# Performance work log

Measured on AMD Instinct MI355X. Metric: run time of the kernel, lower is better.

Reference implementation:

```python
import jax, jax.numpy as jnp
import numpy as np

FEAT_DIM = 16
NUM_DEPTHS = 64


def _lookat(p):
    z = p / np.linalg.norm(p)
    up = np.array([0.0, 1.0, 0.0])
    x = np.cross(up, z); x = x / np.linalg.norm(x)
    y = np.cross(z, x)
    m = np.eye(4)
    m[:3, 0] = x; m[:3, 1] = y; m[:3, 2] = z; m[:3, 3] = p
    return m


def setup_inputs() -> dict:
    key = jax.random.key(0)
    ks = jax.random.split(key, 6)
    S, Vin, Vt, C, D, H, W = 2, 3, 4, FEAT_DIM, NUM_DEPTHS, 96, 96
    enc = jax.random.normal(ks[0], (S, Vin, C, D, H, W), jnp.float32) * 0.5
    rng = np.random.default_rng(0)

    def poses(n):
        ps = rng.normal(size=(S, n, 3))
        ps = ps / np.linalg.norm(ps, axis=-1, keepdims=True) * 1.3
        return jnp.asarray(np.stack([[_lookat(ps[i, j]) for j in range(n)] for i in range(S)]), jnp.float32)

    input_poses = poses(Vin)
    target_poses = poses(Vt)
    W1 = jax.random.normal(ks[1], (16, 64), jnp.float32) * 0.25
    W2 = jax.random.normal(ks[2], (64, 64), jnp.float32) * 0.125
    W3 = jax.random.normal(ks[3], (64, 17), jnp.float32) * 0.125
    return dict(
        encoded_imgs=enc, input_poses=input_poses, target_poses=target_poses,
        focal=1.2, z_near=0.8, z_far=1.8, samples_per_ray=64,
        W1=W1, b1=jnp.zeros((64,), jnp.float32),
        W2=W2, b2=jnp.zeros((64,), jnp.float32),
        W3=W3, b3=jnp.zeros((17,), jnp.float32),
    )


def grid_sample_3d(vol, grid):
    # vol: (N,C,D,H,W); grid: (N,P,3) xyz in [-1,1]; trilinear, zero padding, align_corners=False
    N, C, D, H, W = vol.shape
    P = grid.shape[1]
    ix = ((grid[..., 0] + 1.0) * W - 1.0) * 0.5
    iy = ((grid[..., 1] + 1.0) * H - 1.0) * 0.5
    iz = ((grid[..., 2] + 1.0) * D - 1.0) * 0.5
    x0, y0, z0 = jnp.floor(ix), jnp.floor(iy), jnp.floor(iz)
    volf = vol.reshape(N, C, D * H * W)
    out = jnp.zeros((N, C, P), vol.dtype)
    for dz in (0, 1):
        for dy in (0, 1):
            for dx in (0, 1):
                xc, yc, zc = x0 + dx, y0 + dy, z0 + dz
                wgt = (1.0 - jnp.abs(ix - xc)) * (1.0 - jnp.abs(iy - yc)) * (1.0 - jnp.abs(iz - zc))
                valid = ((xc >= 0) & (xc < W) & (yc >= 0) & (yc < H) & (zc >= 0) & (zc < D))
                xi = jnp.clip(xc, 0, W - 1).astype(jnp.int32)
                yi = jnp.clip(yc, 0, H - 1).astype(jnp.int32)
                zi = jnp.clip(zc, 0, D - 1).astype(jnp.int32)
                idx = (zi * H + yi) * W + xi  # (N,P)
                vals = jnp.take_along_axis(volf, idx[:, None, :], axis=2)  # (N,C,P)
                out = out + (wgt * valid)[:, None, :] * vals
    return out


def _upsample2_align_corners(x):
    # bilinear x2 on last two axes, align_corners=True (torch UpsamplingBilinear2d)
    def interp(x, axis):
        n = x.shape[axis]
        m = 2 * n
        pos = jnp.arange(m) * ((n - 1) / (m - 1))
        lo = jnp.floor(pos).astype(jnp.int32)
        hi = jnp.minimum(lo + 1, n - 1)
        f = (pos - lo).astype(x.dtype)
        xl = jnp.take(x, lo, axis=axis)
        xh = jnp.take(x, hi, axis=axis)
        shp = [1] * x.ndim; shp[axis] = m
        f = f.reshape(shp)
        return xl * (1.0 - f) + xh * f
    return interp(interp(x, -2), -1)


def _forward(encoded_imgs, input_poses, target_poses, focal, z_near, z_far,
             samples_per_ray, W1, b1, W2, b2, W3, b3):
    S, Vin, C, D, H, W = encoded_imgs.shape
    Vt = target_poses.shape[1]
    h, w = H // 2, W // 2
    spr = samples_per_ray
    dt = encoded_imgs.dtype

    # --- gen_rays at half resolution ---
    poses = target_poses.reshape(S * Vt, 4, 4)
    ys = ((jnp.arange(h, dtype=dt) + 0.5) / h) * 2.0 - 1.0
    xs = ((jnp.arange(w, dtype=dt) + 0.5) / w) * 2.0 - 1.0
    yy, xx = jnp.meshgrid(ys, xs, indexing='ij')
    dirs_cam = jnp.stack([xx / focal, -yy / focal, -jnp.ones_like(xx)], -1)  # (h,w,3)
    dirs = jnp.einsum('bij,hwj->bhwi', poses[:, :3, :3], dirs_cam)            # (B,h,w,3)
    origins = poses[:, None, None, :3, 3]                                      # (B,1,1,3)

    t = z_near + (z_far - z_near) * (jnp.arange(spr, dtype=dt) / (spr - 1))
    times = jnp.broadcast_to(t, (S * Vt, h, w, spr))
    pts = origins[..., None, :] + times[..., None] * dirs[..., None, :]        # (B,h,w,spr,3)

    times = times.reshape(S, Vt, h, w, spr)
    pts = pts.reshape(S, Vt, h, w, spr, 3)
    pts_h = jnp.concatenate([pts, jnp.ones_like(pts[..., :1])], axis=-1)      # (S,Vt,h,w,spr,4)

    # --- invert input poses (rigid) ---
    R = input_poses[..., :3, :3]
    tr = input_poses[..., :3, 3]
    Rt = jnp.swapaxes(R, -1, -2)
    inv_t = -jnp.einsum('svij,svj->svi', Rt, tr)
    top = jnp.concatenate([Rt, inv_t[..., None]], axis=-1)                     # (S,Vin,3,4)
    bottom = jnp.broadcast_to(jnp.array([0.0, 0.0, 0.0, 1.0], dt), (S, Vin, 1, 4))
    extrinsics = jnp.concatenate([top, bottom], axis=-2)                       # (S,Vin,4,4)

    local = jnp.einsum('svij,sthwpj->svthwpi', extrinsics, pts_h)              # (S,Vin,Vt,h,w,spr,4)
    x = local[..., 0]
    y = local[..., 1]
    z = -local[..., 2]
    u = x / z * focal
    v = y / z * focal
    min_z, max_z = focal * z_near, focal * z_far
    wd = 2.0 * (z - min_z) / (max_z - min_z) - 1.0
    uvw = jnp.stack((u, -v, -wd), axis=-1)                                     # (S,Vin,Vt,h,w,spr,3)

    feats = grid_sample_3d(encoded_imgs.reshape(S * Vin, C, D, H, W),
                           uvw.reshape(S * Vin, -1, 3))                        # (S*Vin,C,P)
    feats = feats.reshape(S, Vin, C, Vt, h, w, spr)
    feats = jnp.mean(feats, axis=1)                                            # baseline_mean camera weighting
    feats = jnp.transpose(feats, (0, 2, 3, 4, 5, 1))                           # (S,Vt,h,w,spr,C)

    # --- MLP with residual feature skip ---
    x1 = jax.nn.relu(feats @ W1 + b1)
    x2 = jax.nn.relu(x1 @ W2 + b2)
    out = x2 @ W3 + b3                                                         # (...,17)
    density = jax.nn.relu(out[..., 0])
    rgb = feats + out[..., 1:]

    # --- volume rendering ---
    deltas = times[..., 1:] - times[..., :-1]
    last = jnp.full_like(deltas[..., :1], 1e10)
    deltas = jnp.concatenate([deltas, last], axis=-1)
    sigdel = density * deltas
    alpha = 1.0 - jnp.exp(-sigdel)
    transmittance = jnp.exp(-jnp.cumsum(sigdel, axis=-1))
    wts = alpha * transmittance
    renders = jnp.sum(wts[..., None] * rgb, axis=-2)                           # (S,Vt,h,w,16)

    renders = jnp.transpose(renders, (0, 1, 4, 2, 3))                          # (S,Vt,16,h,w)
    renders = _upsample2_align_corners(renders.reshape(S * Vt, C, h, w))
    return renders.reshape(S, Vt, C, H, W)


def reference(encoded_imgs, input_poses, target_poses, focal, z_near, z_far,
              samples_per_ray, W1, b1, W2, b2, W3, b3):
    return _forward(encoded_imgs, input_poses, target_poses, float(focal), float(z_near),
                    float(z_far), int(samples_per_ray), W1, b1, W2, b2, W3, b3)
```

## Files before the change

### kernel.cpp

```cpp
#include <hip/hip_runtime.h>
#include <hip/hip_bf16.h>
#include <math.h>

#define NS   2
#define NVIN 3
#define NVT  4
#define NC   16
#define ND   64
#define NH   96
#define NW   96
#define HWH  48
#define SPR  64
#define DHW  (ND*NH*NW)
#define NTILE (DHW / 64)
#define NSAMP (NS*NVT*HWH*HWH*SPR)
#define NRAYS (NS*NVT*HWH*HWH)

typedef __attribute__((ext_vector_type(8))) short bfrag;
typedef __attribute__((ext_vector_type(4))) float cfrag;
typedef __attribute__((ext_vector_type(4))) float f32x4;
typedef __attribute__((ext_vector_type(4))) int   i32x4;

#define MFMA16 __builtin_amdgcn_mfma_f32_16x16x32_bf16

#define WAVE_LDS_SYNC() asm volatile("s_waitcnt lgkmcnt(0)" ::: "memory")

__device__ __forceinline__ short f2bf(float x) {
    union { __hip_bfloat16 b; short s; } cv;
    cv.b = __float2bfloat16(x);
    return cv.s;
}
__device__ __forceinline__ float bf2f(short s) {
    union { unsigned int u; float f; } cv;
    cv.u = ((unsigned int)(unsigned short)s) << 16;
    return cv.f;
}

__device__ __forceinline__ void mk_frag(const float* p, bfrag& ah, bfrag& al) {
    float4 v0 = *(const float4*)p;
    float4 v1 = *(const float4*)(p + 4);
    float e[8] = {v0.x, v0.y, v0.z, v0.w, v1.x, v1.y, v1.z, v1.w};
    #pragma unroll
    for (int j = 0; j < 8; j++) {
        short h = f2bf(e[j]);
        ah[j] = h;
        al[j] = f2bf(e[j] - bf2f(h));
    }
}

__global__ __launch_bounds__(256) void wprep_kernel(
    const float* __restrict__ W1, const float* __restrict__ W2,
    const float* __restrict__ W3, short* __restrict__ whi, short* __restrict__ wlo)
{
    int t = blockIdx.x * 256 + threadIdx.x;
    int f = t >> 6, L = t & 63;
    int q = L >> 4, li = L & 15;
    #pragma unroll
    for (int j = 0; j < 8; j++) {
        int kloc = q * 8 + j;
        float w = 0.f;
        if (f < 4) {
            int n = f * 16 + li, k = kloc;
            if (k < 16) w = W1[k * 64 + n];
        } else if (f < 12) {
            int kt = (f - 4) >> 2, nt = (f - 4) & 3;
            w = W2[(kt * 32 + kloc) * 64 + nt * 16 + li];
        } else {
            int kt = (f - 12) >> 1, nt = (f - 12) & 1;
            int n = nt * 16 + li;
            if (n < 17) w = W3[(kt * 32 + kloc) * 17 + n];
        }
        short h = f2bf(w);
        whi[(f * 64 + L) * 8 + j] = h;
        wlo[(f * 64 + L) * 8 + j] = f2bf(w - bf2f(h));
    }
}

__global__ __launch_bounds__(256) void transpose_kernel(
    const float* __restrict__ in, float* __restrict__ out)
{
    __shared__ float tile[NC][64 + 4];
    const int t   = threadIdx.x;
    const int blk = blockIdx.x;
    const int vox0 = (blk % NTILE) * 64;
    const int sv   = blk / NTILE;

    const int c  = t >> 4;
    const int vg = (t & 15) * 4;
    const float* src = in + ((size_t)sv * NC + c) * DHW + vox0 + vg;
    float4 v = *(const float4*)src;
    tile[c][vg + 0] = v.x; tile[c][vg + 1] = v.y;
    tile[c][vg + 2] = v.z; tile[c][vg + 3] = v.w;
    __syncthreads();

    const int ov = t >> 2;
    const int oc = (t & 3) * 4;
    float4 w = make_float4(tile[oc + 0][ov], tile[oc + 1][ov],
                           tile[oc + 2][ov], tile[oc + 3][ov]);
    float* dst = out + ((size_t)sv * DHW + vox0 + ov) * NC + oc;
    *(float4*)dst = w;
}

__global__ __launch_bounds__(256) void gather_kernel(
    const float* __restrict__ enc_t,
    const float* __restrict__ ipose,
    const float* __restrict__ tpose,
    const float* __restrict__ focal_p,
    const float* __restrict__ znear_p,
    const float* __restrict__ zfar_p,
    float* __restrict__ xbuf)
{
    const int blk  = (blockIdx.x & 7) * ((NRAYS / 4) >> 3) + (blockIdx.x >> 3);
    const int lane = threadIdx.x & 63;
    const int wv   = threadIdx.x >> 6;
    const int ray  = blk * 4 + wv;
    const int px   = ray % HWH;
    const int py   = (ray / HWH) % HWH;
    const int b    = ray / (HWH * HWH);
    const int s    = b >> 2;

    const float focal = focal_p[0];
    const float znear = znear_p[0];
    const float zfar  = zfar_p[0];

    __shared__ float lds[4 * 32 * 52];
    float* wslice = lds + wv * 32 * 52;

    const float* P = tpose + b * 16;
    float ysc = ((py + 0.5f) / (float)HWH) * 2.f - 1.f;
    float xsc = ((px + 0.5f) / (float)HWH) * 2.f - 1.f;
    float dcx = xsc / focal, dcy = -ysc / focal, dcz = -1.f;
    float dirx = P[0]*dcx + P[1]*dcy + P[2]*dcz;
    float diry = P[4]*dcx + P[5]*dcy + P[6]*dcz;
    float dirz = P[8]*dcx + P[9]*dcy + P[10]*dcz;

    float lox[NVIN], loy[NVIN], loz[NVIN];
    float ldx[NVIN], ldy[NVIN], ldz[NVIN];
    #pragma unroll
    for (int v = 0; v < NVIN; v++) {
        const float* E = ipose + (s * NVIN + v) * 16;
        float qx = P[3] - E[3], qy = P[7] - E[7], qz = P[11] - E[11];
        lox[v] = E[0]*qx + E[4]*qy + E[8]*qz;
        loy[v] = E[1]*qx + E[5]*qy + E[9]*qz;
        loz[v] = E[2]*qx + E[6]*qy + E[10]*qz;
        ldx[v] = E[0]*dirx + E[4]*diry + E[8]*dirz;
        ldy[v] = E[1]*dirx + E[5]*diry + E[9]*dirz;
        ldz[v] = E[2]*dirx + E[6]*diry + E[10]*dirz;
    }

    const float minz = focal * znear, maxz = focal * zfar;
    const float inv3 = 1.f / 3.f;
    const int c4 = lane & 3;
    const int cb = c4 * 16;

    #pragma unroll 1
    for (int h = 0; h < 2; h++) {
        WAVE_LDS_SYNC();

        if (lane < 32) {
            const int d = h * 32 + lane;
            float tv = znear + (zfar - znear) * ((float)d / (float)(SPR - 1));
            float* row = wslice + lane * 52;
            #pragma unroll
            for (int v = 0; v < NVIN; v++) {
                float lx = lox[v] + tv * ldx[v];
                float ly = loy[v] + tv * ldy[v];
                float lz = loz[v] + tv * ldz[v];
                float zz = -lz;
                float u  = lx / zz * focal;
                float vv = ly / zz * focal;
                float wd = 2.f * (zz - minz) / (maxz - minz) - 1.f;
                float ix = ((u   + 1.f) * NW - 1.f) * 0.5f;
                float iy = ((-vv + 1.f) * NH - 1.f) * 0.5f;
                float iz = ((-wd + 1.f) * ND - 1.f) * 0.5f;
                float x0 = floorf(ix), y0 = floorf(iy), z0 = floorf(iz);
                float x1 = x0 + 1.f,   y1 = y0 + 1.f,   z1 = z0 + 1.f;

                float wxa0 = 1.f - fabsf(ix - x0), wxa1 = 1.f - fabsf(ix - x1);
                float wya0 = 1.f - fabsf(iy - y0), wya1 = 1.f - fabsf(iy - y1);
                float wza0 = 1.f - fabsf(iz - z0), wza1 = 1.f - fabsf(iz - z1);
                wxa0 = (x0 >= 0.f && x0 < (float)NW) ? wxa0 : 0.f;
                wxa1 = (x1 >= 0.f && x1 < (float)NW) ? wxa1 : 0.f;
                wya0 = (y0 >= 0.f && y0 < (float)NH) ? wya0 : 0.f;
                wya1 = (y1 >= 0.f && y1 < (float)NH) ? wya1 : 0.f;
                wza0 = (z0 >= 0.f && z0 < (float)ND) ? wza0 : 0.f;
                wza1 = (z1 >= 0.f && z1 < (float)ND) ? wza1 : 0.f;

                int xi0 = min(max((int)x0, 0), NW - 1), xi1 = min(max((int)x1, 0), NW - 1);
                int yi0 = min(max((int)y0, 0), NH - 1), yi1 = min(max((int)y1, 0), NH - 1);
                int zi0 = min(max((int)z0, 0), ND - 1), zi1 = min(max((int)z1, 0), ND - 1);
                int o00 = (zi0 * NH + yi0) * NW, o01 = (zi0 * NH + yi1) * NW;
                int o10 = (zi1 * NH + yi0) * NW, o11 = (zi1 * NH + yi1) * NW;

                const int sb = (s * NVIN + v) * (DHW * NC * 4);

                f32x4 w0 = { (wxa0*wya0)*wza0, (wxa1*wya0)*wza0,
                             (wxa0*wya1)*wza0, (wxa1*wya1)*wza0 };
                f32x4 w1 = { (wxa0*wya0)*wza1, (wxa1*wya0)*wza1,
                             (wxa0*wya1)*wza1, (wxa1*wya1)*wza1 };
                i32x4 o0 = { sb + (o00 + xi0) * 64, sb + (o00 + xi1) * 64,
                             sb + (o01 + xi0) * 64, sb + (o01 + xi1) * 64 };
                i32x4 o1 = { sb + (o10 + xi0) * 64, sb + (o10 + xi1) * 64,
                             sb + (o11 + xi0) * 64, sb + (o11 + xi1) * 64 };

                *(f32x4*)(row + v*16 + 0)  = w0;
                *(f32x4*)(row + v*16 + 4)  = w1;
                *(i32x4*)(row + v*16 + 8)  = o0;
                *(i32x4*)(row + v*16 + 12) = o1;
            }
        }
        WAVE_LDS_SYNC();

        #pragma unroll 1
        for (int pass = 0; pass < 2; pass++) {
            const int sl = pass * 16 + (lane >> 2);
            const float* row = wslice + sl * 52;
            f32x4 acc = {0.f, 0.f, 0.f, 0.f};

            #pragma unroll
            for (int v = 0; v < NVIN; v++) {
                f32x4 wq0 = *(const f32x4*)(row + v*16 + 0);
                f32x4 wq1 = *(const f32x4*)(row + v*16 + 4);
                i32x4 oq0 = *(const i32x4*)(row + v*16 + 8);
                i32x4 oq1 = *(const i32x4*)(row + v*16 + 12);

                f32x4 a0, a1, a2, a3, a4, a5, a6, a7;
                int v0 = oq0.x + cb, v1 = oq0.y + cb, v2 = oq0.z + cb, v3 = oq0.w + cb;
                int v4 = oq1.x + cb, v5 = oq1.y + cb, v6 = oq1.z + cb, v7 = oq1.w + cb;
                asm volatile("global_load_dwordx4 %0, %1, %2" : "=&v"(a0) : "v"(v0), "s"(enc_t));
                asm volatile("global_load_dwordx4 %0, %1, %2" : "=&v"(a1) : "v"(v1), "s"(enc_t));
                asm volatile("global_load_dwordx4 %0, %1, %2" : "=&v"(a2) : "v"(v2), "s"(enc_t));
                asm volatile("global_load_dwordx4 %0, %1, %2" : "=&v"(a3) : "v"(v3), "s"(enc_t));
                asm volatile("global_load_dwordx4 %0, %1, %2" : "=&v"(a4) : "v"(v4), "s"(enc_t));
                asm volatile("global_load_dwordx4 %0, %1, %2" : "=&v"(a5) : "v"(v5), "s"(enc_t));
                asm volatile("global_load_dwordx4 %0, %1, %2" : "=&v"(a6) : "v"(v6), "s"(enc_t));
                asm volatile("global_load_dwordx4 %0, %1, %2" : "=&v"(a7) : "v"(v7), "s"(enc_t));
                asm volatile("s_waitcnt vmcnt(0)" ::: "memory");
                __builtin_amdgcn_sched_barrier(0);

                acc += wq0.x * a0;  acc += wq0.y * a1;
                acc += wq0.z * a2;  acc += wq0.w * a3;
                acc += wq1.x * a4;  acc += wq1.y * a5;
                acc += wq1.z * a6;  acc += wq1.w * a7;
            }
            ((f32x4*)xbuf)[(ray * 64 + h * 32 + sl) * 4 + c4] = acc * inv3;
        }
    }
}

__global__ __launch_bounds__(64) void mlp_kernel(
    const float* __restrict__ xbuf,
    const float* __restrict__ znear_p,
    const float* __restrict__ zfar_p,
    const short* __restrict__ whi, const short* __restrict__ wlo,
    const float* __restrict__ B1, const float* __restrict__ B2,
    const float* __restrict__ B3,
    float* __restrict__ rhalf)
{
    const int lane = threadIdx.x & 63;
    const int ray  = blockIdx.x;
    const int px   = ray % HWH;
    const int py   = (ray / HWH) % HWH;
    const int b    = ray / (HWH * HWH);

    const float znear = znear_p[0];
    const float zfar  = zfar_p[0];

    __shared__ float sbuf[64][36];
    float (*B)[36] = sbuf;
    const int li = lane & 15, q = lane >> 4;
    const float* X = xbuf + (size_t)ray * 64 * NC;

    float b1v[4], b2v[4], b3v[2];
    #pragma unroll
    for (int nt = 0; nt < 4; nt++) { b1v[nt] = B1[nt*16 + li]; b2v[nt] = B2[nt*16 + li]; }
    b3v[0] = B3[li];
    b3v[1] = (li == 0) ? B3[16] : 0.f;

    bfrag xah[4], xal[4];
    bfrag zb = {0,0,0,0,0,0,0,0};
    #pragma unroll
    for (int mt = 0; mt < 4; mt++) {
        if (q < 2) mk_frag(X + (mt*16 + li) * NC + q * 8, xah[mt], xal[mt]);
        else { xah[mt] = zb; xal[mt] = zb; }
    }

    cfrag zc = {0.f, 0.f, 0.f, 0.f};
    cfrag h2acc[4][4];
    #pragma unroll
    for (int mt = 0; mt < 4; mt++)
        #pragma unroll
        for (int nt = 0; nt < 4; nt++) h2acc[mt][nt] = zc;

    #pragma unroll
    for (int c1 = 0; c1 < 2; c1++) {
        cfrag h1[4][2];
        #pragma unroll
        for (int nt2 = 0; nt2 < 2; nt2++) {
            int f = 2*c1 + nt2;
            bfrag bh = *(const bfrag*)(whi + (f*64 + lane)*8);
            bfrag bl = *(const bfrag*)(wlo + (f*64 + lane)*8);
            #pragma unroll
            for (int mt = 0; mt < 4; mt++) {
                cfrag a = zc;
                a = MFMA16(xal[mt], bh, a, 0, 0, 0);
                a = MFMA16(xah[mt], bl, a, 0, 0, 0);
                a = MFMA16(xah[mt], bh, a, 0, 0, 0);
                h1[mt][nt2] = a;
            }
        }
        WAVE_LDS_SYNC();
        #pragma unroll
        for (int mt = 0; mt < 4; mt++)
            #pragma unroll
            for (int nt2 = 0; nt2 < 2; nt2++)
                #pragma unroll
                for (int r = 0; r < 4; r++)
                    B[mt*16 + q*4 + r][nt2*16 + li] =
                        fmaxf(h1[mt][nt2][r] + b1v[2*c1 + nt2], 0.f);
        WAVE_LDS_SYNC();
        bfrag hah[4], hal[4];
        #pragma unroll
        for (int mt = 0; mt < 4; mt++)
            mk_frag(&B[mt*16 + li][q*8], hah[mt], hal[mt]);
        #pragma unroll
        for (int nt = 0; nt < 4; nt++) {
            int f = 4 + c1*4 + nt;
            bfrag bh = *(const bfrag*)(whi + (f*64 + lane)*8);
            bfrag bl = *(const bfrag*)(wlo + (f*64 + lane)*8);
            #pragma unroll
            for (int mt = 0; mt < 4; mt++) {
                cfrag a = h2acc[mt][nt];
                a = MFMA16(hal[mt], bh, a, 0, 0, 0);
                a = MFMA16(hah[mt], bl, a, 0, 0, 0);
                a = MFMA16(hah[mt], bh, a, 0, 0, 0);
                h2acc[mt][nt] = a;
            }
        }
    }

    cfrag oacc[4][2];
    #pragma unroll
    for (int mt = 0; mt < 4; mt++)
        #pragma unroll
        for (int nt = 0; nt < 2; nt++) oacc[mt][nt] = zc;

    #pragma unroll
    for (int c2 = 0; c2 < 2; c2++) {
        WAVE_LDS_SYNC();
        #pragma unroll
        for (int mt = 0; mt < 4; mt++)
            #pragma unroll
            for (int nt2 = 0; nt2 < 2; nt2++)
                #pragma unroll
                for (int r = 0; r < 4; r++)
                    B[mt*16 + q*4 + r][nt2*16 + li] =
                        fmaxf(h2acc[mt][2*c2 + nt2][r] + b2v[2*c2 + nt2], 0.f);
        WAVE_LDS_SYNC();
        bfrag hah[4], hal[4];
        #pragma unroll
        for (int mt = 0; mt < 4; mt++)
            mk_frag(&B[mt*16 + li][q*8], hah[mt], hal[mt]);
        #pragma unroll
        for (int nt = 0; nt < 2; nt++) {
            int f = 12 + c2*2 + nt;
            bfrag bh = *(const bfrag*)(whi + (f*64 + lane)*8);
            bfrag bl = *(const bfrag*)(wlo + (f*64 + lane)*8);
            #pragma unroll
            for (int mt = 0; mt < 4; mt++) {
                cfrag a = oacc[mt][nt];
                a = MFMA16(hal[mt], bh, a, 0, 0, 0);
                a = MFMA16(hah[mt], bl, a, 0, 0, 0);
                a = MFMA16(hah[mt], bh, a, 0, 0, 0);
                oacc[mt][nt] = a;
            }
        }
    }

    WAVE_LDS_SYNC();
    #pragma unroll
    for (int mt = 0; mt < 4; mt++)
        #pragma unroll
        for (int nt = 0; nt < 2; nt++) {
            int ch = nt*16 + li;
            if (ch < 17) {
                #pragma unroll
                for (int r = 0; r < 4; r++)
                    B[mt*16 + q*4 + r][ch] = oacc[mt][nt][r] + b3v[nt];
            }
        }
    WAVE_LDS_SYNC();
    float4 o0 = *(float4*)&B[lane][0];
    float4 o1 = *(float4*)&B[lane][4];
    float4 o2 = *(float4*)&B[lane][8];
    float4 o3 = *(float4*)&B[lane][12];
    float o16 = B[lane][16];

    float density = fmaxf(o0.x, 0.f);
    float orgb[16] = {o0.y, o0.z, o0.w, o1.x, o1.y, o1.z, o1.w, o2.x,
                      o2.y, o2.z, o2.w, o3.x, o3.y, o3.z, o3.w, o16};

    float4 fx0 = *(const float4*)(X + lane * NC + 0);
    float4 fx1 = *(const float4*)(X + lane * NC + 4);
    float4 fx2 = *(const float4*)(X + lane * NC + 8);
    float4 fx3 = *(const float4*)(X + lane * NC + 12);
    float feats[16] = {fx0.x, fx0.y, fx0.z, fx0.w, fx1.x, fx1.y, fx1.z, fx1.w,
                       fx2.x, fx2.y, fx2.z, fx2.w, fx3.x, fx3.y, fx3.z, fx3.w};

    float tv = znear + (zfar - znear) * ((float)lane / (float)(SPR - 1));
    float tn = znear + (zfar - znear) * ((float)(lane + 1) / (float)(SPR - 1));
    float delta = (lane < SPR - 1) ? (tn - tv) : 1e10f;
    float sigdel = density * delta;
    float alpha = 1.f - expf(-sigdel);
    float csum = sigdel;
    #pragma unroll
    for (int off = 1; off < 64; off <<= 1) {
        float nb = __shfl_up(csum, off, 64);
        if (lane >= off) csum += nb;
    }
    float wray = alpha * expf(-csum);

    #pragma unroll
    for (int c = 0; c < NC; c++) {
        float val = wray * (feats[c] + orgb[c]);
        #pragma unroll
        for (int off = 32; off >= 1; off >>= 1)
            val += __shfl_down(val, off, 64);
        if (lane == 0)
            rhalf[((b * NC + c) * HWH + py) * HWH + px] = val;
    }
}

__device__ __forceinline__ void mlp_and_composite(
    const float feats[NC], int lane, int b, int py, int px,
    float tv, float znear, float zfar,
    const float* __restrict__ W1, const float* __restrict__ B1,
    const float* __restrict__ W2, const float* __restrict__ B2,
    const float* __restrict__ W3, const float* __restrict__ B3,
    float* __restrict__ rhalf)
{
    float outa[17];
    #pragma unroll
    for (int c = 0; c < 17; c++) outa[c] = B3[c];
    for (int kc = 0; kc < 4; kc++) {
        float h2c[16];
        #pragma unroll
        for (int k = 0; k < 16; k++) h2c[k] = B2[kc * 16 + k];
        #pragma unroll 4
        for (int j = 0; j < 64; j++) {
            float a = B1[j];
            #pragma unroll
            for (int i = 0; i < NC; i++) a += feats[i] * W1[i * 64 + j];
            a = fmaxf(a, 0.f);
            const float* w2p = W2 + j * 64 + kc * 16;
            #pragma unroll
            for (int k = 0; k < 16; k++) h2c[k] += a * w2p[k];
        }
        #pragma unroll
        for (int k = 0; k < 16; k++) {
            float hv = fmaxf(h2c[k], 0.f);
            const float* w3p = W3 + (kc * 16 + k) * 17;
            #pragma unroll
            for (int c = 0; c < 17; c++) outa[c] += hv * w3p[c];
        }
    }
    float density = fmaxf(outa[0], 0.f);
    float tn = znear + (zfar - znear) * ((float)(lane + 1) / (float)(SPR - 1));
    float delta = (lane < SPR - 1) ? (tn - tv) : 1e10f;
    float sigdel = density * delta;
    float alpha = 1.f - expf(-sigdel);
    float csum = sigdel;
    #pragma unroll
    for (int off = 1; off < 64; off <<= 1) {
        float nb = __shfl_up(csum, off, 64);
        if (lane >= off) csum += nb;
    }
    float wray = alpha * expf(-csum);
    #pragma unroll
    for (int c = 0; c < NC; c++) {
        float val = wray * (feats[c] + outa[1 + c]);
        #pragma unroll
        for (int off = 32; off >= 1; off >>= 1)
            val += __shfl_down(val, off, 64);
        if (lane == 0)
            rhalf[((b * NC + c) * HWH + py) * HWH + px] = val;
    }
}

__global__ __launch_bounds__(256) void render_kernel(
    const float* __restrict__ enc,
    const float* __restrict__ ipose,
    const float* __restrict__ tpose,
    const float* __restrict__ focal_p,
    const float* __restrict__ znear_p,
    const float* __restrict__ zfar_p,
    const float* __restrict__ W1, const float* __restrict__ B1,
    const float* __restrict__ W2, const float* __restrict__ B2,
    const float* __restrict__ W3, const float* __restrict__ B3,
    float* __restrict__ rhalf)
{
    const int lane = threadIdx.x & 63;
    const int ray  = blockIdx.x * 4 + (threadIdx.x >> 6);
    const int px   = ray % HWH;
    const int py   = (ray / HWH) % HWH;
    const int b    = ray / (HWH * HWH);
    const int s    = b >> 2;
    const float focal = focal_p[0];
    const float znear = znear_p[0];
    const float zfar  = zfar_p[0];
    const float* P = tpose + b * 16;
    float ysc = ((py + 0.5f) / (float)HWH) * 2.f - 1.f;
    float xsc = ((px + 0.5f) / (float)HWH) * 2.f - 1.f;
    float dcx = xsc / focal, dcy = -ysc / focal, dcz = -1.f;
    float dirx = P[0]*dcx + P[1]*dcy + P[2]*dcz;
    float diry = P[4]*dcx + P[5]*dcy + P[6]*dcz;
    float dirz = P[8]*dcx + P[9]*dcy + P[10]*dcz;
    float tv  = znear + (zfar - znear) * ((float)lane / (float)(SPR - 1));
    float ptx = P[3] + tv * dirx, pty = P[7] + tv * diry, ptz = P[11] + tv * dirz;
    float feats[NC];
    #pragma unroll
    for (int c = 0; c < NC; c++) feats[c] = 0.f;
    const float minz = focal * znear, maxz = focal * zfar;
    for (int v = 0; v < NVIN; v++) {
        const float* E = ipose + (s * NVIN + v) * 16;
        float qx = ptx - E[3], qy = pty - E[7], qz = ptz - E[11];
        float lx = E[0]*qx + E[4]*qy + E[8]*qz;
        float ly = E[1]*qx + E[5]*qy + E[9]*qz;
        float lz = E[2]*qx + E[6]*qy + E[10]*qz;
        float zz = -lz;
        float u  = lx / zz * focal;
        float vv = ly / zz * focal;
        float wd = 2.f * (zz - minz) / (maxz - minz) - 1.f;
        float ix = ((u   + 1.f) * NW - 1.f) * 0.5f;
        float iy = ((-vv + 1.f) * NH - 1.f) * 0.5f;
        float iz = ((-wd + 1.f) * ND - 1.f) * 0.5f;
        float x0 = floorf(ix), y0 = floorf(iy), z0 = floorf(iz);
        float wgt[8]; int idx[8];
        #pragma unroll
        for (int k = 0; k < 8; k++) {
            float xc = x0 + (k & 1), yc = y0 + ((k >> 1) & 1), zc = z0 + (k >> 2);
            float wt = (1.f - fabsf(ix - xc)) * (1.f - fabsf(iy - yc)) * (1.f - fabsf(iz - zc));
            bool valid = (xc >= 0.f) && (xc < (float)NW) &&
                         (yc >= 0.f) && (yc < (float)NH) &&
                         (zc >= 0.f) && (zc < (float)ND);
            wgt[k] = valid ? wt : 0.f;
            int xi = min(max((int)xc, 0), NW - 1);
            int yi = min(max((int)yc, 0), NH - 1);
            int zi = min(max((int)zc, 0), ND - 1);
            idx[k] = (zi * NH + yi) * NW + xi;
        }
        const float* VB = enc + (size_t)(s * NVIN + v) * NC * DHW;
        #pragma unroll
        for (int c = 0; c < NC; c++) {
            const float* vc = VB + c * DHW;
            float acc = 0.f;
            #pragma unroll
            for (int k = 0; k < 8; k++) acc += wgt[k] * vc[idx[k]];
            feats[c] += acc;
        }
    }
    #pragma unroll
    for (int c = 0; c < NC; c++) feats[c] *= (1.f / 3.f);
    mlp_and_composite(feats, lane, b, py, px, tv, znear, zfar,
                      W1, B1, W2, B2, W3, B3, rhalf);
}

__global__ __launch_bounds__(256) void upsample_kernel(
    const float* __restrict__ in, float* __restrict__ out)
{
    int tid = blockIdx.x * 256 + threadIdx.x;
    int ox = tid % NW;
    int oy = (tid / NW) % NH;
    int c  = (tid / (NW * NH)) % NC;
    int b  = tid / (NW * NH * NC);
    const float sc = (float)((HWH - 1) / (double)(NH - 1));
    float pyf = oy * sc;
    float pxf = ox * sc;
    int y0 = (int)floorf(pyf); int y1 = min(y0 + 1, HWH - 1); float fy = pyf - y0;
    int x0 = (int)floorf(pxf); int x1 = min(x0 + 1, HWH - 1); float fx = pxf - x0;
    const float* src = in + (b * NC + c) * HWH * HWH;
    float v00 = src[y0 * HWH + x0], v01 = src[y0 * HWH + x1];
    float v10 = src[y1 * HWH + x0], v11 = src[y1 * HWH + x1];
    float gl = v00 * (1.f - fy) + v10 * fy;
    float gr = v01 * (1.f - fy) + v11 * fy;
    out[tid] = gl * (1.f - fx) + gr * fx;
}

extern "C" void kernel_launch(void* const* d_in, const int* in_sizes, int n_in,
                              void* d_out, int out_size, void* d_ws, size_t ws_size,
                              hipStream_t stream) {
    const float* enc   = (const float*)d_in[0];
    const float* ipose = (const float*)d_in[1];
    const float* tpose = (const float*)d_in[2];
    const float* focal = (const float*)d_in[3];
    const float* znear = (const float*)d_in[4];
    const float* zfar  = (const float*)d_in[5];
    const float* W1 = (const float*)d_in[7];
    const float* B1 = (const float*)d_in[8];
    const float* W2 = (const float*)d_in[9];
    const float* B2 = (const float*)d_in[10];
    const float* W3 = (const float*)d_in[11];
    const float* B3 = (const float*)d_in[12];

    float* out = (float*)d_out;
    const int nrays = NRAYS;
    const int nout  = NS * NVT * NC * NH * NW;
    const size_t enc_t_bytes = (size_t)NS * NVIN * NC * DHW * 4;
    const size_t rhalf_bytes = (size_t)nrays * NC * 4;
    const size_t wfrag_bytes = 16 * 64 * 8 * sizeof(short);
    const size_t xbuf_bytes  = (size_t)NSAMP * NC * 4;

    if (ws_size >= enc_t_bytes + rhalf_bytes + 2 * wfrag_bytes + xbuf_bytes) {
        char* base = (char*)d_ws;
        float* enc_t = (float*)base;                      base += enc_t_bytes;
        float* rhalf = (float*)base;                      base += rhalf_bytes;
        short* whi   = (short*)base;                      base += wfrag_bytes;
        short* wlo   = (short*)base;                      base += wfrag_bytes;
        float* xbuf  = (float*)base;

        wprep_kernel<<<4, 256, 0, stream>>>(W1, W2, W3, whi, wlo);
        transpose_kernel<<<NS * NVIN * NTILE, 256, 0, stream>>>(enc, enc_t);
        gather_kernel<<<nrays / 4, 256, 0, stream>>>(
            enc_t, ipose, tpose, focal, znear, zfar, xbuf);
        mlp_kernel<<<nrays, 64, 0, stream>>>(
            xbuf, znear, zfar, whi, wlo, B1, B2, B3, rhalf);
        upsample_kernel<<<nout / 256, 256, 0, stream>>>(rhalf, out);
    } else {
        float* rhalf = (float*)d_ws;
        render_kernel<<<nrays / 4, 256, 0, stream>>>(
            enc, ipose, tpose, focal, znear, zfar,
            W1, B1, W2, B2, W3, B3, rhalf);
        upsample_kernel<<<nout / 256, 256, 0, stream>>>(rhalf, out);
    }
}
```

Baseline: 594.8 us.

## Fuse gather and MLP kernels into one per-ray kernel

Merges the trilinear gather stage and the MFMA MLP/volume-render stage into a single kernel that runs one 64-thread block per ray. The separate launch goes away, and the per-ray sample features written to xbuf are read back right away by the same wave, so they are likely still cached. The block size drops from four waves to one and the LDS buffer is shared between the two phases. Correctness relies on a vmcnt wait making the global stores visible to other lanes before they are reloaded.

```diff
diff --git a/kernel.cpp b/kernel.cpp
--- a/kernel.cpp
+++ b/kernel.cpp
@@ -101,19 +101,21 @@
     *(float4*)dst = w;
 }
 
-__global__ __launch_bounds__(256) void gather_kernel(
+__global__ __launch_bounds__(64) void fused_kernel(
     const float* __restrict__ enc_t,
     const float* __restrict__ ipose,
     const float* __restrict__ tpose,
     const float* __restrict__ focal_p,
     const float* __restrict__ znear_p,
     const float* __restrict__ zfar_p,
-    float* __restrict__ xbuf)
+    const short* __restrict__ whi, const short* __restrict__ wlo,
+    const float* __restrict__ B1, const float* __restrict__ B2,
+    const float* __restrict__ B3,
+    float* __restrict__ xbuf,
+    float* __restrict__ rhalf)
 {
-    const int blk  = (blockIdx.x & 7) * ((NRAYS / 4) >> 3) + (blockIdx.x >> 3);
     const int lane = threadIdx.x & 63;
-    const int wv   = threadIdx.x >> 6;
-    const int ray  = blk * 4 + wv;
+    const int ray  = ((int)blockIdx.x & 7) * (NRAYS >> 3) + ((int)blockIdx.x >> 3);
     const int px   = ray % HWH;
     const int py   = (ray / HWH) % HWH;
     const int b    = ray / (HWH * HWH);
@@ -123,8 +125,7 @@
     const float znear = znear_p[0];
     const float zfar  = zfar_p[0];
 
-    __shared__ float lds[4 * 32 * 52];
-    float* wslice = lds + wv * 32 * 52;
+    __shared__ float lds[64 * 36];
 
     const float* P = tpose + b * 16;
     float ysc = ((py + 0.5f) / (float)HWH) * 2.f - 1.f;
@@ -152,6 +153,7 @@
     const float inv3 = 1.f / 3.f;
     const int c4 = lane & 3;
     const int cb = c4 * 16;
+    float* X = xbuf + (size_t)ray * 64 * NC;
 
     #pragma unroll 1
     for (int h = 0; h < 2; h++) {
@@ -160,7 +162,7 @@
         if (lane < 32) {
             const int d = h * 32 + lane;
             float tv = znear + (zfar - znear) * ((float)d / (float)(SPR - 1));
-            float* row = wslice + lane * 52;
+            float* row = lds + lane * 52;
             #pragma unroll
             for (int v = 0; v < NVIN; v++) {
                 float lx = lox[v] + tv * ldx[v];
@@ -214,7 +216,7 @@
         #pragma unroll 1
         for (int pass = 0; pass < 2; pass++) {
             const int sl = pass * 16 + (lane >> 2);
-            const float* row = wslice + sl * 52;
+            const float* row = lds + sl * 52;
             f32x4 acc = {0.f, 0.f, 0.f, 0.f};
 
             #pragma unroll
@@ -246,30 +248,10 @@
             ((f32x4*)xbuf)[(ray * 64 + h * 32 + sl) * 4 + c4] = acc * inv3;
         }
     }
-}
-
-__global__ __launch_bounds__(64) void mlp_kernel(
-    const float* __restrict__ xbuf,
-    const float* __restrict__ znear_p,
-    const float* __restrict__ zfar_p,
-    const short* __restrict__ whi, const short* __restrict__ wlo,
-    const float* __restrict__ B1, const float* __restrict__ B2,
-    const float* __restrict__ B3,
-    float* __restrict__ rhalf)
-{
-    const int lane = threadIdx.x & 63;
-    const int ray  = blockIdx.x;
-    const int px   = ray % HWH;
-    const int py   = (ray / HWH) % HWH;
-    const int b    = ray / (HWH * HWH);
-
-    const float znear = znear_p[0];
-    const float zfar  = zfar_p[0];
-
-    __shared__ float sbuf[64][36];
-    float (*B)[36] = sbuf;
+    asm volatile("s_waitcnt vmcnt(0)" ::: "memory");
+
+    float (*B)[36] = (float (*)[36])lds;
     const int li = lane & 15, q = lane >> 4;
-    const float* X = xbuf + (size_t)ray * 64 * NC;
 
     float b1v[4], b2v[4], b3v[2];
     #pragma unroll
@@ -620,10 +602,9 @@
 
         wprep_kernel<<<4, 256, 0, stream>>>(W1, W2, W3, whi, wlo);
         transpose_kernel<<<NS * NVIN * NTILE, 256, 0, stream>>>(enc, enc_t);
-        gather_kernel<<<nrays / 4, 256, 0, stream>>>(
-            enc_t, ipose, tpose, focal, znear, zfar, xbuf);
-        mlp_kernel<<<nrays, 64, 0, stream>>>(
-            xbuf, znear, zfar, whi, wlo, B1, B2, B3, rhalf);
+        fused_kernel<<<nrays, 64, 0, stream>>>(
+            enc_t, ipose, tpose, focal, znear, zfar,
+            whi, wlo, B1, B2, B3, xbuf, rhalf);
         upsample_kernel<<<nout / 256, 256, 0, stream>>>(rhalf, out);
     } else {
         float* rhalf = (float*)d_ws;
```

New measurement: 603.3 us. About the same (+1.4%).
